# Kernel optimization log

Measured on AMD Instinct MI355X. Metric: run time of the kernel, lower is better.

Reference implementation:

```python
import jax, jax.numpy as jnp
import numpy as np

EMBED = 1024
HEADS = 16
HEAD_DIM = EMBED // HEADS


def setup_inputs() -> dict:
    key = jax.random.key(0)
    ks = jax.random.split(key, 10)
    s = 1.0 / np.sqrt(EMBED)
    inp = {
        "x": jax.random.normal(ks[0], (4, 2048, EMBED), dtype=jnp.float32),
        "mask": jax.random.randint(ks[1], (4, 2048), 0, 2, dtype=jnp.int32),
        "Wq": jax.random.uniform(ks[2], (EMBED, EMBED), jnp.float32, -s, s),
        "bq": jax.random.uniform(ks[3], (EMBED,), jnp.float32, -s, s),
        "Wk": jax.random.uniform(ks[4], (EMBED, EMBED), jnp.float32, -s, s),
        "bk": jax.random.uniform(ks[5], (EMBED,), jnp.float32, -s, s),
        "Wv": jax.random.uniform(ks[6], (EMBED, EMBED), jnp.float32, -s, s),
        "bv": jax.random.uniform(ks[7], (EMBED,), jnp.float32, -s, s),
        "Wo": jax.random.uniform(ks[8], (EMBED, EMBED), jnp.float32, -s, s),
        "bo": jax.random.uniform(ks[9], (EMBED,), jnp.float32, -s, s),
    }
    return inp


def reference(x, mask, Wq, bq, Wk, bk, Wv, bv, Wo, bo):
    B, S, E = x.shape
    scale = np.sqrt(HEAD_DIM).astype(np.float32)

    def split_heads(t):  # [B,S,E] -> [B,H,S,D]
        return t.reshape(B, S, HEADS, HEAD_DIM).transpose(0, 2, 1, 3)

    Q = split_heads(x @ Wq.T + bq)
    K = split_heads(x @ Wk.T + bk)
    V = split_heads(x @ Wv.T + bv)

    scores = jnp.einsum("bhqd,bhkd->bhqk", Q, K) / scale  # [B,H,S,S]
    # mask [B,S] broadcast over heads and query dim (key-padding mask)
    scores = jnp.where(mask[:, None, None, :] == 0, -jnp.inf, scores)
    weights = jax.nn.softmax(scores, axis=-1)
    out = jnp.einsum("bhqk,bhkd->bhqd", weights, V)  # [B,H,S,D]
    out = out.transpose(0, 2, 1, 3).reshape(B, S, E)
    return out @ Wo.T + bo
```

## Files before the change

kernel.cpp:

```cpp
#include <hip/hip_runtime.h>

#define BATCH 4
#define SEQ   2048
#define EMBED 1024
#define HEADS 16
#define HDIM  64
#define NTOK  (BATCH*SEQ)
#define VROWS 72

typedef __attribute__((ext_vector_type(8)))  short short8;
typedef __attribute__((ext_vector_type(4)))  float f32x4;
typedef __attribute__((ext_vector_type(16))) float f32x16;

static __device__ __forceinline__ unsigned short f2bf(float f) {
    union { float f; unsigned u; } v; v.f = f;
    return (unsigned short)((v.u + 0x7FFFu + ((v.u >> 16) & 1u)) >> 16);
}
static __device__ __forceinline__ unsigned pk2bf(float lo, float hi) {
    union { float f; unsigned u; } a, b; a.f = lo; b.f = hi;
    return __builtin_amdgcn_perm(b.u + 0x8000u, a.u + 0x8000u, 0x07060302u);
}
static __device__ __forceinline__ void gload_lds16(const unsigned short* g, unsigned short* l) {
    __builtin_amdgcn_global_load_lds(
        (__attribute__((address_space(1))) void*)g,
        (__attribute__((address_space(3))) void*)l, 16, 0, 0);
}

#define SCQ 0.180336880f

__global__ void cast_all(const float* __restrict__ x,
                         const float* __restrict__ w0, const float* __restrict__ w1,
                         const float* __restrict__ w2, const float* __restrict__ w3,
                         unsigned short* __restrict__ xb,
                         unsigned short* __restrict__ wb)
{
    const int bid = blockIdx.x;
    const float* src;
    unsigned short* dst;
    int i;
    if (bid < 4096) {
        src = x; dst = xb; i = (bid * 256 + threadIdx.x) * 8;
    } else {
        const int wz = (bid - 4096) >> 9;
        const float* ws[4] = {w0, w1, w2, w3};
        src = ws[wz];
        dst = wb + (size_t)wz * (EMBED * EMBED);
        i = (((bid - 4096) & 511) * 256 + threadIdx.x) * 8;
    }
    float4 a = *(const float4*)(src + i);
    float4 b = *(const float4*)(src + i + 4);
    union { int4 v; unsigned short u[8]; } pk;
    pk.u[0] = f2bf(a.x); pk.u[1] = f2bf(a.y); pk.u[2] = f2bf(a.z); pk.u[3] = f2bf(a.w);
    pk.u[4] = f2bf(b.x); pk.u[5] = f2bf(b.y); pk.u[6] = f2bf(b.z); pk.u[7] = f2bf(b.w);
    *(int4*)(dst + i) = pk.v;
}

__global__ void maskrow(const int* __restrict__ mask, unsigned short* __restrict__ VtG)
{
    const int idx = blockIdx.x * 256 + threadIdx.x;
    const int s  = idx & (SEQ - 1);
    const int bh = idx >> 11;
    const int b  = bh >> 4;
    const unsigned short mv = mask[b * SEQ + s] ? (unsigned short)0x3F80 : (unsigned short)0;
    const size_t base = (size_t)bh * VROWS * SEQ + s;
#pragma unroll
    for (int r = 64; r < 72; ++r)
        VtG[base + (size_t)r * SEQ] = (r == 64 || r == 68) ? mv : (unsigned short)0;
}

__global__ __launch_bounds__(256, 2)
void gemm_qkv(const unsigned short* __restrict__ Xb,
              const unsigned short* __restrict__ Wall,
              const float* __restrict__ bq, const float* __restrict__ bk,
              const float* __restrict__ bv, const int* __restrict__ mask,
              unsigned short* __restrict__ Qw, unsigned short* __restrict__ Kw,
              unsigned short* __restrict__ VtG)
{
    __shared__ unsigned short Ws[3][128][32];
    __shared__ unsigned short Xs[128][32];

    const int tid  = threadIdx.x;
    const int f0   = blockIdx.x * 128;
    const int t0   = blockIdx.y * 128;
    const int lane = tid & 63, m = lane & 15, quad = lane >> 4;
    const int wid  = tid >> 6;
    const int wf   = (wid & 1) * 64;
    const int wt   = (wid >> 1) * 64;

    const int r    = tid >> 2, cc = tid & 3, sw = (tid >> 4) & 3;
    const int gcol = (cc ^ sw) << 3;
    const unsigned short* Xp = Xb + (size_t)(t0 + r) * EMBED + gcol;
    const unsigned short* Wp = Wall + (size_t)(f0 + r) * EMBED + gcol;
    unsigned short* XsL = &Xs[0][0] + tid * 8;
    unsigned short* WsL = &Ws[0][0][0] + tid * 8;

    const int qs = (quad ^ ((m >> 2) & 3)) << 3;

    f32x4 aq[4][4] = {}, ak[4][4] = {}, av[4][4] = {};

    for (int k0 = 0; k0 < EMBED; k0 += 32) {
        __syncthreads();
        gload_lds16(Xp + k0,              XsL);
        gload_lds16(Xp + k0 + 64 * EMBED, XsL + 2048);
#pragma unroll
        for (int z = 0; z < 3; ++z) {
            const unsigned short* wz = Wp + (size_t)z * EMBED * EMBED + k0;
            gload_lds16(wz,              WsL + z * 4096);
            gload_lds16(wz + 64 * EMBED, WsL + z * 4096 + 2048);
        }
        __syncthreads();

        short8 bf4[4];
#pragma unroll
        for (int nb = 0; nb < 4; ++nb)
            bf4[nb] = *(const short8*)&Xs[wt + nb * 16 + m][qs];

#pragma unroll
        for (int z = 0; z < 3; ++z) {
            short8 af[4];
#pragma unroll
            for (int mb = 0; mb < 4; ++mb)
                af[mb] = *(const short8*)&Ws[z][wf + mb * 16 + m][qs];
            f32x4 (&acc)[4][4] = (z == 0) ? aq : (z == 1) ? ak : av;
#pragma unroll
            for (int mb = 0; mb < 4; ++mb)
#pragma unroll
                for (int nb = 0; nb < 4; ++nb)
                    acc[mb][nb] = __builtin_amdgcn_mfma_f32_16x16x32_bf16(
                        af[mb], bf4[nb], acc[mb][nb], 0, 0, 0);
        }
    }

#pragma unroll
    for (int mb = 0; mb < 4; ++mb) {
        const int feat = f0 + wf + mb * 16 + quad * 4;
        float4 bv4 = *(const float4*)&bq[feat];
#pragma unroll
        for (int nb = 0; nb < 4; ++nb) {
            const int tok = t0 + wt + nb * 16 + m;
            ushort4 pk;
            pk.x = f2bf((aq[mb][nb][0] + bv4.x) * SCQ);
            pk.y = f2bf((aq[mb][nb][1] + bv4.y) * SCQ);
            pk.z = f2bf((aq[mb][nb][2] + bv4.z) * SCQ);
            pk.w = f2bf((aq[mb][nb][3] + bv4.w) * SCQ);
            *(ushort4*)(Qw + (size_t)tok * EMBED + feat) = pk;
        }
    }
#pragma unroll
    for (int mb = 0; mb < 4; ++mb) {
        const int feat = f0 + wf + mb * 16 + quad * 4;
        float4 bv4 = *(const float4*)&bk[feat];
#pragma unroll
        for (int nb = 0; nb < 4; ++nb) {
            const int tok = t0 + wt + nb * 16 + m;
            ushort4 pk;
            pk.x = f2bf(ak[mb][nb][0] + bv4.x);
            pk.y = f2bf(ak[mb][nb][1] + bv4.y);
            pk.z = f2bf(ak[mb][nb][2] + bv4.z);
            pk.w = f2bf(ak[mb][nb][3] + bv4.w);
            *(ushort4*)(Kw + (size_t)tok * EMBED + feat) = pk;
        }
    }
    {
        const int h = (f0 + wf) >> 6;
#pragma unroll
        for (int nb = 0; nb < 4; ++nb) {
            const int tok = t0 + wt + nb * 16 + m;
            const int b   = tok >> 11;
            const int s   = tok & (SEQ - 1);
            const float mf = mask[tok] ? 1.f : 0.f;
            const size_t base = ((size_t)(b * HEADS + h) * VROWS) * SEQ + s;
#pragma unroll
            for (int mb = 0; mb < 4; ++mb) {
                const int feat  = f0 + wf + mb * 16 + quad * 4;
                const int dbase = mb * 16 + quad * 4;
                float4 bv4 = *(const float4*)&bv[feat];
                VtG[base + (size_t)(dbase + 0) * SEQ] = f2bf((av[mb][nb][0] + bv4.x) * mf);
                VtG[base + (size_t)(dbase + 1) * SEQ] = f2bf((av[mb][nb][1] + bv4.y) * mf);
                VtG[base + (size_t)(dbase + 2) * SEQ] = f2bf((av[mb][nb][2] + bv4.z) * mf);
                VtG[base + (size_t)(dbase + 3) * SEQ] = f2bf((av[mb][nb][3] + bv4.w) * mf);
            }
        }
    }
}

__global__ __launch_bounds__(256, 4)
void attn_mfma(const unsigned short* __restrict__ Qb,
               const unsigned short* __restrict__ Kb,
               const unsigned short* __restrict__ VtG,
               unsigned short* __restrict__ Ob)
{
    __shared__ unsigned short Ks[64][72];
    __shared__ unsigned short Vs[96][72];

    const int tid  = threadIdx.x;
    const int bid  = blockIdx.x;
    const int qb   = bid & 15;
    const int h    = (bid >> 4) & 15;
    const int b    = bid >> 8;
    const int wid  = tid >> 6, lane = tid & 63;
    const int q32  = lane & 31, hi = lane >> 5;
    const int tb   = b * SEQ;
    const int q    = qb * 128 + wid * 32 + q32;

    const unsigned short* qrow = Qb + (size_t)(tb + q) * EMBED + h * HDIM;
    short8 qf[4];
#pragma unroll
    for (int st = 0; st < 4; ++st)
        qf[st] = *(const short8*)(qrow + st * 16 + hi * 8);

    f32x16 o0, o1, o2, z16;
#pragma unroll
    for (int i = 0; i < 16; ++i) { z16[i] = 0.f; }
    o0 = z16; o1 = z16; o2 = z16;

    {
        int* vz = (int*)&Vs[72][0];
        for (int i = tid; i < 864; i += 256) vz[i] = 0;
    }

    const int sr = tid >> 2, sc = (tid & 3) * 16;
    const unsigned short* kSrc = Kb + (size_t)(tb + sr) * EMBED + h * HDIM + sc;
    const size_t vhead = (size_t)(b * HEADS + h) * VROWS;
    const unsigned short* vSrc = VtG + (vhead + sr) * SEQ + sc;
    const unsigned short* vSrc2 = VtG + (vhead + 64 + (tid >> 2)) * SEQ + (tid & 3) * 16;

    for (int kt = 0; kt < SEQ; kt += 64) {
        int4 kv0 = *(const int4*)(kSrc + (size_t)kt * EMBED);
        int4 kv1 = *(const int4*)(kSrc + (size_t)kt * EMBED + 8);
        int4 vv0 = *(const int4*)(vSrc + kt);
        int4 vv1 = *(const int4*)(vSrc + kt + 8);
        int4 mv0, mv1;
        if (tid < 32) { mv0 = *(const int4*)(vSrc2 + kt); mv1 = *(const int4*)(vSrc2 + kt + 8); }
        __syncthreads();
        *(int4*)&Ks[sr][sc]     = kv0;
        *(int4*)&Ks[sr][sc + 8] = kv1;
        *(int4*)&Vs[sr][sc]     = vv0;
        *(int4*)&Vs[sr][sc + 8] = vv1;
        if (tid < 32) {
            *(int4*)&Vs[64 + (tid >> 2)][(tid & 3) * 16]     = mv0;
            *(int4*)&Vs[64 + (tid >> 2)][(tid & 3) * 16 + 8] = mv1;
        }
        __syncthreads();

#pragma unroll
        for (int kb = 0; kb < 2; ++kb) {
            f32x16 s = z16;
#pragma unroll
            for (int st = 0; st < 4; ++st) {
                short8 kf = *(const short8*)&Ks[kb * 32 + q32][st * 16 + hi * 8];
                s = __builtin_amdgcn_mfma_f32_32x32x16_bf16(kf, qf[st], s, 0, 0, 0);
            }

            float p[16];
#pragma unroll
            for (int i = 0; i < 16; ++i) p[i] = __builtin_amdgcn_exp2f(s[i]);
            unsigned D[8];
#pragma unroll
            for (int j = 0; j < 8; ++j) D[j] = pk2bf(p[2 * j], p[2 * j + 1]);

#pragma unroll
            for (int cl = 0; cl < 2; ++cl) {
                unsigned s0 = hi ? D[4 * cl + 0] : D[4 * cl + 2];
                unsigned s1 = hi ? D[4 * cl + 1] : D[4 * cl + 3];
                unsigned r0 = (unsigned)__shfl_xor((int)s0, 32);
                unsigned r1 = (unsigned)__shfl_xor((int)s1, 32);
                union { uint4 u; short8 s8; } fr;
                fr.u.x = hi ? r0 : D[4 * cl + 0];
                fr.u.y = hi ? r1 : D[4 * cl + 1];
                fr.u.z = hi ? D[4 * cl + 2] : r0;
                fr.u.w = hi ? D[4 * cl + 3] : r1;

                const int kcol = kb * 32 + cl * 16 + hi * 8;
                short8 vf0 = *(const short8*)&Vs[q32][kcol];
                short8 vf1 = *(const short8*)&Vs[32 + q32][kcol];
                short8 vf2 = *(const short8*)&Vs[64 + q32][kcol];
                o0 = __builtin_amdgcn_mfma_f32_32x32x16_bf16(vf0, fr.s8, o0, 0, 0, 0);
                o1 = __builtin_amdgcn_mfma_f32_32x32x16_bf16(vf1, fr.s8, o1, 0, 0, 0);
                o2 = __builtin_amdgcn_mfma_f32_32x32x16_bf16(vf2, fr.s8, o2, 0, 0, 0);
            }
        }
    }

    const float inv = 1.0f / o2[0];
    unsigned short* orow = Ob + (size_t)(tb + q) * EMBED + h * HDIM;
#pragma unroll
    for (int db = 0; db < 2; ++db) {
        const f32x16& oo = db ? o1 : o0;
#pragma unroll
        for (int qg = 0; qg < 4; ++qg) {
            ushort4 pk;
            pk.x = f2bf(oo[qg * 4 + 0] * inv);
            pk.y = f2bf(oo[qg * 4 + 1] * inv);
            pk.z = f2bf(oo[qg * 4 + 2] * inv);
            pk.w = f2bf(oo[qg * 4 + 3] * inv);
            *(ushort4*)(orow + db * 32 + qg * 8 + hi * 4) = pk;
        }
    }
}

__global__ __launch_bounds__(256, 2)
void gemm_o(const unsigned short* __restrict__ W, const unsigned short* __restrict__ X,
            const float* __restrict__ bias, float* __restrict__ Cout)
{
    __shared__ unsigned short Ws[128][32];
    __shared__ unsigned short Xs[128][32];

    const int tid  = threadIdx.x;
    const int f0   = blockIdx.x * 128;
    const int t0   = blockIdx.y * 128;
    const int lane = tid & 63, m = lane & 15, quad = lane >> 4;
    const int wid  = tid >> 6;
    const int wf   = (wid & 1) * 64;
    const int wt   = (wid >> 1) * 64;

    const int r    = tid >> 2, cc = tid & 3, sw = (tid >> 4) & 3;
    const int gcol = (cc ^ sw) << 3;
    const unsigned short* Wp = W + (size_t)(f0 + r) * EMBED + gcol;
    const unsigned short* Xp = X + (size_t)(t0 + r) * EMBED + gcol;
    unsigned short* WsL = &Ws[0][0] + tid * 8;
    unsigned short* XsL = &Xs[0][0] + tid * 8;

    const int qs = (quad ^ ((m >> 2) & 3)) << 3;

    f32x4 acc[4][4] = {};

    for (int k0 = 0; k0 < EMBED; k0 += 32) {
        __syncthreads();
        gload_lds16(Wp + k0,              WsL);
        gload_lds16(Wp + k0 + 64 * EMBED, WsL + 2048);
        gload_lds16(Xp + k0,              XsL);
        gload_lds16(Xp + k0 + 64 * EMBED, XsL + 2048);
        __syncthreads();

        short8 af[4], bf4[4];
#pragma unroll
        for (int mb = 0; mb < 4; ++mb)
            af[mb] = *(const short8*)&Ws[wf + mb * 16 + m][qs];
#pragma unroll
        for (int nb = 0; nb < 4; ++nb)
            bf4[nb] = *(const short8*)&Xs[wt + nb * 16 + m][qs];
#pragma unroll
        for (int mb = 0; mb < 4; ++mb)
#pragma unroll
            for (int nb = 0; nb < 4; ++nb)
                acc[mb][nb] = __builtin_amdgcn_mfma_f32_16x16x32_bf16(
                    af[mb], bf4[nb], acc[mb][nb], 0, 0, 0);
    }

#pragma unroll
    for (int mb = 0; mb < 4; ++mb) {
        const int feat = f0 + wf + mb * 16 + quad * 4;
        float4 bv4 = *(const float4*)&bias[feat];
#pragma unroll
        for (int nb = 0; nb < 4; ++nb) {
            const int tok = t0 + wt + nb * 16 + m;
            float4 st;
            st.x = acc[mb][nb][0] + bv4.x;
            st.y = acc[mb][nb][1] + bv4.y;
            st.z = acc[mb][nb][2] + bv4.z;
            st.w = acc[mb][nb][3] + bv4.w;
            *(float4*)(Cout + (size_t)tok * EMBED + feat) = st;
        }
    }
}

extern "C" void kernel_launch(void* const* d_in, const int* in_sizes, int n_in,
                              void* d_out, int out_size, void* d_ws, size_t ws_size,
                              hipStream_t stream)
{
    const float* x    = (const float*)d_in[0];
    const int*   mask = (const int*)  d_in[1];
    const float* Wq   = (const float*)d_in[2];
    const float* bq   = (const float*)d_in[3];
    const float* Wk   = (const float*)d_in[4];
    const float* bk   = (const float*)d_in[5];
    const float* Wv   = (const float*)d_in[6];
    const float* bv   = (const float*)d_in[7];
    const float* Wo   = (const float*)d_in[8];
    const float* bo   = (const float*)d_in[9];
    float* out = (float*)d_out;

    const size_t NE = (size_t)NTOK * EMBED;
    const size_t WE = (size_t)EMBED * EMBED;
    const size_t VE = (size_t)BATCH * HEADS * VROWS * SEQ;
    unsigned short* Xb  = (unsigned short*)d_ws;
    unsigned short* Wqb = Xb + NE;
    unsigned short* Wob = Wqb + 3 * WE;
    unsigned short* Qw  = Wob + WE;
    unsigned short* Kw  = Qw + NE;
    unsigned short* VtG = Kw + NE;
    unsigned short* Ow  = Xb;

    cast_all<<<4096 + 2048, 256, 0, stream>>>(x, Wq, Wk, Wv, Wo, Xb, Wqb);

    maskrow<<<(BATCH * HEADS * SEQ) / 256, 256, 0, stream>>>(mask, VtG);

    gemm_qkv<<<dim3(8, 64), 256, 0, stream>>>(Xb, Wqb, bq, bk, bv, mask, Qw, Kw, VtG);

    attn_mfma<<<BATCH * HEADS * (SEQ / 128), 256, 0, stream>>>(Qw, Kw, VtG, Ow);

    gemm_o<<<dim3(8, 64), 256, 0, stream>>>(Wob, Ow, bo, out);
}
```

Before: 286.9 us.

## Double-buffer attention K/V tiles, apply mask via MFMA bias, drop maskrow kernel

The attention kernel now double-buffers K/V tiles in LDS and prefetches the next tile into registers, so only one barrier is needed per iteration. The key-padding mask is read directly and added as a large negative bias through an extra rank-1 MFMA. The row sum is accumulated in registers instead of through a third PV MFMA over extra V rows, which removes the maskrow kernel and the padded V rows. The GEMM and attention kernels also remap block indices for better L2 locality. The cost is one extra MFMA per score tile, more LDS, and reliance on exp2 of a large negative value underflowing to zero.

```diff
diff --git a/kernel.cpp b/kernel.cpp
--- a/kernel.cpp
+++ b/kernel.cpp
@@ -6,7 +6,6 @@
 #define HEADS 16
 #define HDIM  64
 #define NTOK  (BATCH*SEQ)
-#define VROWS 72
 
 typedef __attribute__((ext_vector_type(8)))  short short8;
 typedef __attribute__((ext_vector_type(4)))  float f32x4;
@@ -55,24 +54,11 @@
     *(int4*)(dst + i) = pk.v;
 }
 
-__global__ void maskrow(const int* __restrict__ mask, unsigned short* __restrict__ VtG)
-{
-    const int idx = blockIdx.x * 256 + threadIdx.x;
-    const int s  = idx & (SEQ - 1);
-    const int bh = idx >> 11;
-    const int b  = bh >> 4;
-    const unsigned short mv = mask[b * SEQ + s] ? (unsigned short)0x3F80 : (unsigned short)0;
-    const size_t base = (size_t)bh * VROWS * SEQ + s;
-#pragma unroll
-    for (int r = 64; r < 72; ++r)
-        VtG[base + (size_t)r * SEQ] = (r == 64 || r == 68) ? mv : (unsigned short)0;
-}
-
 __global__ __launch_bounds__(256, 2)
 void gemm_qkv(const unsigned short* __restrict__ Xb,
               const unsigned short* __restrict__ Wall,
               const float* __restrict__ bq, const float* __restrict__ bk,
-              const float* __restrict__ bv, const int* __restrict__ mask,
+              const float* __restrict__ bv,
               unsigned short* __restrict__ Qw, unsigned short* __restrict__ Kw,
               unsigned short* __restrict__ VtG)
 {
@@ -80,8 +66,9 @@
     __shared__ unsigned short Xs[128][32];
 
     const int tid  = threadIdx.x;
-    const int f0   = blockIdx.x * 128;
-    const int t0   = blockIdx.y * 128;
+    const int bx   = blockIdx.x, by = blockIdx.y;
+    const int f0   = (by >> 3) * 128;
+    const int t0   = ((bx << 3) | (by & 7)) * 128;
     const int lane = tid & 63, m = lane & 15, quad = lane >> 4;
     const int wid  = tid >> 6;
     const int wf   = (wid & 1) * 64;
@@ -168,17 +155,16 @@
             const int tok = t0 + wt + nb * 16 + m;
             const int b   = tok >> 11;
             const int s   = tok & (SEQ - 1);
-            const float mf = mask[tok] ? 1.f : 0.f;
-            const size_t base = ((size_t)(b * HEADS + h) * VROWS) * SEQ + s;
+            const size_t base = ((size_t)(b * HEADS + h) * HDIM) * SEQ + s;
 #pragma unroll
             for (int mb = 0; mb < 4; ++mb) {
                 const int feat  = f0 + wf + mb * 16 + quad * 4;
                 const int dbase = mb * 16 + quad * 4;
                 float4 bv4 = *(const float4*)&bv[feat];
-                VtG[base + (size_t)(dbase + 0) * SEQ] = f2bf((av[mb][nb][0] + bv4.x) * mf);
-                VtG[base + (size_t)(dbase + 1) * SEQ] = f2bf((av[mb][nb][1] + bv4.y) * mf);
-                VtG[base + (size_t)(dbase + 2) * SEQ] = f2bf((av[mb][nb][2] + bv4.z) * mf);
-                VtG[base + (size_t)(dbase + 3) * SEQ] = f2bf((av[mb][nb][3] + bv4.w) * mf);
+                VtG[base + (size_t)(dbase + 0) * SEQ] = f2bf(av[mb][nb][0] + bv4.x);
+                VtG[base + (size_t)(dbase + 1) * SEQ] = f2bf(av[mb][nb][1] + bv4.y);
+                VtG[base + (size_t)(dbase + 2) * SEQ] = f2bf(av[mb][nb][2] + bv4.z);
+                VtG[base + (size_t)(dbase + 3) * SEQ] = f2bf(av[mb][nb][3] + bv4.w);
             }
         }
     }
@@ -188,16 +174,17 @@
 void attn_mfma(const unsigned short* __restrict__ Qb,
                const unsigned short* __restrict__ Kb,
                const unsigned short* __restrict__ VtG,
+               const int* __restrict__ mask,
                unsigned short* __restrict__ Ob)
 {
-    __shared__ unsigned short Ks[64][72];
-    __shared__ unsigned short Vs[96][72];
+    __shared__ unsigned short Ks[2][64][72];
+    __shared__ unsigned short Vs[2][64][72];
 
     const int tid  = threadIdx.x;
-    const int bid  = blockIdx.x;
-    const int qb   = bid & 15;
-    const int h    = (bid >> 4) & 15;
-    const int b    = bid >> 8;
+    const int lin  = (blockIdx.x & 7) * 128 + (blockIdx.x >> 3);
+    const int qb   = lin & 15;
+    const int h    = (lin >> 4) & 15;
+    const int b    = lin >> 8;
     const int wid  = tid >> 6, lane = tid & 63;
     const int q32  = lane & 31, hi = lane >> 5;
     const int tb   = b * SEQ;
@@ -209,52 +196,67 @@
     for (int st = 0; st < 4; ++st)
         qf[st] = *(const short8*)(qrow + st * 16 + hi * 8);
 
-    f32x16 o0, o1, o2, z16;
+    short8 mqf = {0, 0, 0, 0, 0, 0, 0, 0};
+    mqf[0] = hi ? (short)0 : (short)0xC480;
+
+    f32x16 o0, o1, z16;
 #pragma unroll
     for (int i = 0; i < 16; ++i) { z16[i] = 0.f; }
-    o0 = z16; o1 = z16; o2 = z16;
-
-    {
-        int* vz = (int*)&Vs[72][0];
-        for (int i = tid; i < 864; i += 256) vz[i] = 0;
-    }
+    o0 = z16; o1 = z16;
+    float lr = 0.f;
 
     const int sr = tid >> 2, sc = (tid & 3) * 16;
     const unsigned short* kSrc = Kb + (size_t)(tb + sr) * EMBED + h * HDIM + sc;
-    const size_t vhead = (size_t)(b * HEADS + h) * VROWS;
-    const unsigned short* vSrc = VtG + (vhead + sr) * SEQ + sc;
-    const unsigned short* vSrc2 = VtG + (vhead + 64 + (tid >> 2)) * SEQ + (tid & 3) * 16;
-
-    for (int kt = 0; kt < SEQ; kt += 64) {
-        int4 kv0 = *(const int4*)(kSrc + (size_t)kt * EMBED);
-        int4 kv1 = *(const int4*)(kSrc + (size_t)kt * EMBED + 8);
-        int4 vv0 = *(const int4*)(vSrc + kt);
-        int4 vv1 = *(const int4*)(vSrc + kt + 8);
-        int4 mv0, mv1;
-        if (tid < 32) { mv0 = *(const int4*)(vSrc2 + kt); mv1 = *(const int4*)(vSrc2 + kt + 8); }
+    const unsigned short* vSrc = VtG + ((size_t)(b * HEADS + h) * HDIM + sr) * SEQ + sc;
+    const int* mrow = mask + b * SEQ;
+
+    int4 kv0 = *(const int4*)(kSrc);
+    int4 kv1 = *(const int4*)(kSrc + 8);
+    int4 vv0 = *(const int4*)(vSrc);
+    int4 vv1 = *(const int4*)(vSrc + 8);
+    int mva = mrow[q32];
+    int mvb = mrow[32 + q32];
+
+    int cur = 0;
+    for (int kt = 0; kt < SEQ; kt += 64, cur ^= 1) {
+        *(int4*)&Ks[cur][sr][sc]     = kv0;
+        *(int4*)&Ks[cur][sr][sc + 8] = kv1;
+        *(int4*)&Vs[cur][sr][sc]     = vv0;
+        *(int4*)&Vs[cur][sr][sc + 8] = vv1;
         __syncthreads();
-        *(int4*)&Ks[sr][sc]     = kv0;
-        *(int4*)&Ks[sr][sc + 8] = kv1;
-        *(int4*)&Vs[sr][sc]     = vv0;
-        *(int4*)&Vs[sr][sc + 8] = vv1;
-        if (tid < 32) {
-            *(int4*)&Vs[64 + (tid >> 2)][(tid & 3) * 16]     = mv0;
-            *(int4*)&Vs[64 + (tid >> 2)][(tid & 3) * 16 + 8] = mv1;
-        }
-        __syncthreads();
+
+        short8 mkfa = {0, 0, 0, 0, 0, 0, 0, 0};
+        short8 mkfb = {0, 0, 0, 0, 0, 0, 0, 0};
+        mkfa[0] = (hi == 0 && mva == 0) ? (short)0x3F80 : (short)0;
+        mkfb[0] = (hi == 0 && mvb == 0) ? (short)0x3F80 : (short)0;
+
+        const int ktn = kt + 64;
+        if (ktn < SEQ) {
+            kv0 = *(const int4*)(kSrc + (size_t)ktn * EMBED);
+            kv1 = *(const int4*)(kSrc + (size_t)ktn * EMBED + 8);
+            vv0 = *(const int4*)(vSrc + ktn);
+            vv1 = *(const int4*)(vSrc + ktn + 8);
+            mva = mrow[ktn + q32];
+            mvb = mrow[ktn + 32 + q32];
+        }
 
 #pragma unroll
         for (int kb = 0; kb < 2; ++kb) {
-            f32x16 s = z16;
+            f32x16 s = __builtin_amdgcn_mfma_f32_32x32x16_bf16(
+                kb ? mkfb : mkfa, mqf, z16, 0, 0, 0);
 #pragma unroll
             for (int st = 0; st < 4; ++st) {
-                short8 kf = *(const short8*)&Ks[kb * 32 + q32][st * 16 + hi * 8];
+                short8 kf = *(const short8*)&Ks[cur][kb * 32 + q32][st * 16 + hi * 8];
                 s = __builtin_amdgcn_mfma_f32_32x32x16_bf16(kf, qf[st], s, 0, 0, 0);
             }
 
             float p[16];
 #pragma unroll
             for (int i = 0; i < 16; ++i) p[i] = __builtin_amdgcn_exp2f(s[i]);
+
+            lr += (((p[0] + p[1]) + (p[2] + p[3])) + ((p[4] + p[5]) + (p[6] + p[7])))
+                + (((p[8] + p[9]) + (p[10] + p[11])) + ((p[12] + p[13]) + (p[14] + p[15])));
+
             unsigned D[8];
 #pragma unroll
             for (int j = 0; j < 8; ++j) D[j] = pk2bf(p[2 * j], p[2 * j + 1]);
@@ -272,17 +274,16 @@
                 fr.u.w = hi ? D[4 * cl + 3] : r1;
 
                 const int kcol = kb * 32 + cl * 16 + hi * 8;
-                short8 vf0 = *(const short8*)&Vs[q32][kcol];
-                short8 vf1 = *(const short8*)&Vs[32 + q32][kcol];
-                short8 vf2 = *(const short8*)&Vs[64 + q32][kcol];
+                short8 vf0 = *(const short8*)&Vs[cur][q32][kcol];
+                short8 vf1 = *(const short8*)&Vs[cur][32 + q32][kcol];
                 o0 = __builtin_amdgcn_mfma_f32_32x32x16_bf16(vf0, fr.s8, o0, 0, 0, 0);
                 o1 = __builtin_amdgcn_mfma_f32_32x32x16_bf16(vf1, fr.s8, o1, 0, 0, 0);
-                o2 = __builtin_amdgcn_mfma_f32_32x32x16_bf16(vf2, fr.s8, o2, 0, 0, 0);
             }
         }
     }
 
-    const float inv = 1.0f / o2[0];
+    const float lrt = lr + __shfl_xor(lr, 32);
+    const float inv = 1.0f / lrt;
     unsigned short* orow = Ob + (size_t)(tb + q) * EMBED + h * HDIM;
 #pragma unroll
     for (int db = 0; db < 2; ++db) {
@@ -307,8 +308,9 @@
     __shared__ unsigned short Xs[128][32];
 
     const int tid  = threadIdx.x;
-    const int f0   = blockIdx.x * 128;
-    const int t0   = blockIdx.y * 128;
+    const int bx   = blockIdx.x, by = blockIdx.y;
+    const int f0   = (by >> 3) * 128;
+    const int t0   = ((bx << 3) | (by & 7)) * 128;
     const int lane = tid & 63, m = lane & 15, quad = lane >> 4;
     const int wid  = tid >> 6;
     const int wf   = (wid & 1) * 64;
@@ -383,7 +385,6 @@
 
     const size_t NE = (size_t)NTOK * EMBED;
     const size_t WE = (size_t)EMBED * EMBED;
-    const size_t VE = (size_t)BATCH * HEADS * VROWS * SEQ;
     unsigned short* Xb  = (unsigned short*)d_ws;
     unsigned short* Wqb = Xb + NE;
     unsigned short* Wob = Wqb + 3 * WE;
@@ -394,11 +395,9 @@
 
     cast_all<<<4096 + 2048, 256, 0, stream>>>(x, Wq, Wk, Wv, Wo, Xb, Wqb);
 
-    maskrow<<<(BATCH * HEADS * SEQ) / 256, 256, 0, stream>>>(mask, VtG);
-
-    gemm_qkv<<<dim3(8, 64), 256, 0, stream>>>(Xb, Wqb, bq, bk, bv, mask, Qw, Kw, VtG);
-
-    attn_mfma<<<BATCH * HEADS * (SEQ / 128), 256, 0, stream>>>(Qw, Kw, VtG, Ow);
+    gemm_qkv<<<dim3(8, 64), 256, 0, stream>>>(Xb, Wqb, bq, bk, bv, Qw, Kw, VtG);
+
+    attn_mfma<<<BATCH * HEADS * (SEQ / 128), 256, 0, stream>>>(Qw, Kw, VtG, mask, Ow);
 
     gemm_o<<<dim3(8, 64), 256, 0, stream>>>(Wob, Ow, bo, out);
 }
```

Result: slower. 311.2 us (+8.5%).
